# Performance work log

Measured on AMD Instinct MI355X. Metric: run time of the kernel, lower is better.

Reference implementation:

```python
import jax, jax.numpy as jnp
import numpy as np

B, S, IN, OUT = 4, 2048, 4096, 16384

def setup_inputs() -> dict:
    key = jax.random.key(0)
    k1, k2, k3, k4 = jax.random.split(key, 4)
    x = jax.random.normal(k1, (B, S, IN), dtype=jnp.float32)
    quantized_weight = jax.random.randint(k2, (OUT, IN), 0, 16, dtype=jnp.int32)
    scale = jax.random.uniform(k3, (OUT,), dtype=jnp.float32)
    zero_point = jax.random.randint(k4, (OUT,), 0, 16, dtype=jnp.int32)
    return {"x": x, "quantized_weight": quantized_weight, "scale": scale, "zero_point": zero_point}

def reference(x, quantized_weight, scale, zero_point):
    # Per-output-channel dequantization: W = (q - zp) * scale, shape [OUT, IN]
    weight = (quantized_weight.astype(jnp.float32) - zero_point.astype(jnp.float32)[:, None]) * scale[:, None]
    # F.linear(x, W) = x @ W.T -> [B, S, OUT]
    return jnp.einsum('bsi,oi->bso', x, weight)
```

## Files before the change

### kernel.cpp

```cpp
#include <hip/hip_runtime.h>
#include <stdint.h>

#define MDIM 8192
#define NDIM 16384
#define KDIM 4096
#define NT   64
#define PSTR 1048576

typedef __attribute__((ext_vector_type(4)))  int i32x4;
typedef __attribute__((ext_vector_type(16))) int i32x16;

__device__ __forceinline__ void gload_lds16(const void* g, void* l) {
    __builtin_amdgcn_global_load_lds(
        (const __attribute__((address_space(1))) void*)g,
        (__attribute__((address_space(3))) void*)l,
        16, 0, 0);
}

__device__ __forceinline__ i32x16 MFMA32(i32x4 a, i32x4 b, i32x16 c) {
    return __builtin_amdgcn_mfma_i32_32x32x32_i8(a, b, c, 0, 0, 0);
}


__global__ __launch_bounds__(256)
void rowmax_kernel(const float* __restrict__ x, float* __restrict__ sx,
                   float* __restrict__ invx) {
    const int row = (int)blockIdx.x;
    const float4* xr = (const float4*)(x + (long)row * KDIM);
    const int t = threadIdx.x;
    float m = 0.f;
#pragma unroll
    for (int i = 0; i < 4; ++i) {
        float4 v = xr[t + 256 * i];
        m = fmaxf(m, fmaxf(fmaxf(fabsf(v.x), fabsf(v.y)), fmaxf(fabsf(v.z), fabsf(v.w))));
    }
#pragma unroll
    for (int off = 32; off >= 1; off >>= 1) m = fmaxf(m, __shfl_xor(m, off));
    __shared__ float red[4];
    if ((t & 63) == 0) red[t >> 6] = m;
    __syncthreads();
    m = fmaxf(fmaxf(red[0], red[1]), fmaxf(red[2], red[3]));
    m = fmaxf(m, 1e-20f);
    if (t == 0) { sx[row] = m * (1.0f / 127.0f); invx[row] = 127.0f / m; }
}

__global__ __launch_bounds__(256)
void quantx_t2(const float* __restrict__ x, const float* __restrict__ invx,
               int8_t* __restrict__ xq) {
    __shared__ int4 tb[1024];
    const int b = (int)blockIdx.x;
    const int p = b >> 6, tt = b & 63;
    const int tid = threadIdx.x;
#pragma unroll
    for (int i = 0; i < 4; ++i) {
        const int idx = i * 256 + tid;
        const int row = idx >> 2, c = idx & 3;
        const float inv = invx[p * 256 + row];
        const float4* src = (const float4*)(x + ((long)p * 256 + row) * KDIM + tt * 64 + c * 16);
        union { int8_t ch[16]; int4 v; } r;
#pragma unroll
        for (int j = 0; j < 4; ++j) {
            float4 v = src[j];
            r.ch[j * 4 + 0] = (int8_t)__float2int_rn(v.x * inv);
            r.ch[j * 4 + 1] = (int8_t)__float2int_rn(v.y * inv);
            r.ch[j * 4 + 2] = (int8_t)__float2int_rn(v.z * inv);
            r.ch[j * 4 + 3] = (int8_t)__float2int_rn(v.w * inv);
        }
        tb[c * 256 + row] = r.v;
    }
    __syncthreads();
    int4* dst = (int4*)(xq + (long)p * PSTR + (long)tt * 16384);
#pragma unroll
    for (int i = 0; i < 4; ++i) {
        const int idx = i * 256 + tid;
        dst[idx] = tb[idx];
    }
}

__global__ __launch_bounds__(256)
void quantw_t2(const int* __restrict__ q, const int* __restrict__ zp,
               int8_t* __restrict__ wq) {
    __shared__ int4 tb[1024];
    const int b = (int)blockIdx.x;
    const int p = b >> 6, tt = b & 63;
    const int tid = threadIdx.x;
#pragma unroll
    for (int i = 0; i < 4; ++i) {
        const int idx = i * 256 + tid;
        const int row = idx >> 2, c = idx & 3;
        const int z = zp[p * 256 + row];
        const int4* src = (const int4*)(q + ((long)p * 256 + row) * KDIM + tt * 64 + c * 16);
        union { int8_t ch[16]; int4 v; } r;
#pragma unroll
        for (int j = 0; j < 4; ++j) {
            int4 a = src[j];
            r.ch[j * 4 + 0] = (int8_t)(a.x - z);
            r.ch[j * 4 + 1] = (int8_t)(a.y - z);
            r.ch[j * 4 + 2] = (int8_t)(a.z - z);
            r.ch[j * 4 + 3] = (int8_t)(a.w - z);
        }
        tb[c * 256 + row] = r.v;
    }
    __syncthreads();
    int4* dst = (int4*)(wq + (long)p * PSTR + (long)tt * 16384);
#pragma unroll
    for (int i = 0; i < 4; ++i) {
        const int idx = i * 256 + tid;
        dst[idx] = tb[idx];
    }
}


__global__ __launch_bounds__(256, 2)
void gemm_i8_kernel(const int8_t* __restrict__ A, const int8_t* __restrict__ Wt,
                    const float* __restrict__ scale, const float* __restrict__ sx,
                    float* __restrict__ C) {
    __shared__ int8_t lds[2][16384];

    const int wg  = (int)blockIdx.x;
    const int rr  = wg >> 9;
    const int ii  = wg & 511;
    const int bm2 = ii & 63;
    const int bn2 = rr * 8 + (ii >> 6);

    const int tid  = threadIdx.x;
    const int lane = tid & 63;
    const int wid  = tid >> 6;
    const int wm   = wid >> 1;
    const int wn   = wid & 1;
    const int l31  = lane & 31;
    const int lh   = lane >> 5;

    const int fA = lh * 2048 + (wm * 64 + l31) * 16;
    const int fB = 8192 + lh * 2048 + (wn * 64 + l31) * 16;

    const int s0 = tid, s1 = tid + 256;
    const int g0 = (s0 >> 7) * 4096 + (s0 & 127) * 16;
    const int g1 = (s1 >> 7) * 4096 + (s1 & 127) * 16;

    const int8_t* pA = A  + (long)(bm2 >> 1) * PSTR + (bm2 & 1) * 2048;
    const int8_t* pB = Wt + (long)(bn2 >> 1) * PSTR + (bn2 & 1) * 2048;

#define STAGE(BUF, TT)                                                              \
    do {                                                                            \
        const int ko_ = (TT) * 16384;                                               \
        gload_lds16(pA + ko_ + g0, &lds[BUF][s0 * 16]);                             \
        gload_lds16(pA + ko_ + g1, &lds[BUF][s1 * 16]);                             \
        gload_lds16(pB + ko_ + g0, &lds[BUF][8192 + s0 * 16]);                      \
        gload_lds16(pB + ko_ + g1, &lds[BUF][8192 + s1 * 16]);                      \
    } while (0)

    i32x16 acc[2][2];
#pragma unroll
    for (int i = 0; i < 2; ++i)
#pragma unroll
        for (int j = 0; j < 2; ++j)
#pragma unroll
            for (int r = 0; r < 16; ++r) acc[i][j][r] = 0;

    STAGE(0, 0);
    asm volatile("s_waitcnt vmcnt(0)" ::: "memory");
    __builtin_amdgcn_s_barrier();

    for (int t = 0; t < NT; ++t) {
        const int cur = t & 1;
        const bool pf = (t + 1 < NT);
        if (pf) STAGE(cur ^ 1, t + 1);

        i32x4 aF[4], bF[4];
#pragma unroll
        for (int mt = 0; mt < 2; ++mt)
#pragma unroll
            for (int ks = 0; ks < 2; ++ks)
                aF[mt * 2 + ks] = *(const i32x4*)&lds[cur][fA + ks * 4096 + mt * 512];
#pragma unroll
        for (int nt = 0; nt < 2; ++nt)
#pragma unroll
            for (int ks = 0; ks < 2; ++ks)
                bF[nt * 2 + ks] = *(const i32x4*)&lds[cur][fB + ks * 4096 + nt * 512];

        __builtin_amdgcn_s_setprio(1);
#pragma unroll
        for (int mt = 0; mt < 2; ++mt)
#pragma unroll
            for (int nt = 0; nt < 2; ++nt)
#pragma unroll
                for (int ks = 0; ks < 2; ++ks)
                    acc[mt][nt] = MFMA32(aF[mt * 2 + ks], bF[nt * 2 + ks], acc[mt][nt]);
        __builtin_amdgcn_s_setprio(0);

        asm volatile("s_waitcnt lgkmcnt(0)" ::: "memory");
        if (pf) asm volatile("s_waitcnt vmcnt(0)" ::: "memory");
        __builtin_amdgcn_s_barrier();
    }
#undef STAGE

    const long rowA0 = (long)bm2 * 128 + wm * 64;
    const int  colB0 = bn2 * 128 + wn * 64;
    float scj[2];
#pragma unroll
    for (int n = 0; n < 2; ++n) scj[n] = scale[colB0 + n * 32 + l31];
#pragma unroll
    for (int mt = 0; mt < 2; ++mt) {
#pragma unroll
        for (int g = 0; g < 4; ++g) {
            const long rb = rowA0 + mt * 32 + g * 8 + lh * 4;
            const float4 s4 = *(const float4*)(sx + rb);
#pragma unroll
            for (int n = 0; n < 2; ++n) {
                float* cp = C + rb * NDIM + colB0 + n * 32 + l31;
                cp[0 * (long)NDIM] = (float)acc[mt][n][g * 4 + 0] * scj[n] * s4.x;
                cp[1 * (long)NDIM] = (float)acc[mt][n][g * 4 + 1] * scj[n] * s4.y;
                cp[2 * (long)NDIM] = (float)acc[mt][n][g * 4 + 2] * scj[n] * s4.z;
                cp[3 * (long)NDIM] = (float)acc[mt][n][g * 4 + 3] * scj[n] * s4.w;
            }
        }
    }
}


__global__ __launch_bounds__(256)
void fallback_kernel(const float* __restrict__ x, const int* __restrict__ q,
                     const float* __restrict__ scale, const int* __restrict__ zp,
                     float* __restrict__ out) {
    __shared__ float sA[64][17];
    __shared__ float sB[64][17];
    const int bn = (int)blockIdx.x % (NDIM / 64);
    const int bm = (int)blockIdx.x / (NDIM / 64);
    const int t  = threadIdx.x;
    const int tx = t & 15, ty = t >> 4;
    const long rowA = (long)bm * 64, rowB = (long)bn * 64;
    float acc[4][4] = {};
    for (int k0 = 0; k0 < KDIM; k0 += 16) {
#pragma unroll
        for (int i = 0; i < 4; ++i) {
            const int e = t + i * 256;
            const int r = e >> 4, c = e & 15;
            sA[r][c] = x[(rowA + r) * KDIM + k0 + c];
            const int o = (int)rowB + r;
            sB[r][c] = (float)(q[(long)o * KDIM + k0 + c] - zp[o]) * scale[o];
        }
        __syncthreads();
#pragma unroll
        for (int kk = 0; kk < 16; ++kk) {
            float a[4], b[4];
#pragma unroll
            for (int i = 0; i < 4; ++i) a[i] = sA[ty * 4 + i][kk];
#pragma unroll
            for (int j = 0; j < 4; ++j) b[j] = sB[tx * 4 + j][kk];
#pragma unroll
            for (int i = 0; i < 4; ++i)
#pragma unroll
                for (int j = 0; j < 4; ++j) acc[i][j] += a[i] * b[j];
        }
        __syncthreads();
    }
#pragma unroll
    for (int i = 0; i < 4; ++i) {
        const long r = rowA + ty * 4 + i;
#pragma unroll
        for (int j = 0; j < 4; ++j)
            out[r * NDIM + rowB + tx * 4 + j] = acc[i][j];
    }
}


extern "C" void kernel_launch(void* const* d_in, const int* in_sizes, int n_in,
                              void* d_out, int out_size, void* d_ws, size_t ws_size,
                              hipStream_t stream) {
    const float* x     = (const float*)d_in[0];
    const int*   qw    = (const int*)d_in[1];
    const float* scale = (const float*)d_in[2];
    const int*   zp    = (const int*)d_in[3];
    float*       out   = (float*)d_out;

    const size_t needA  = (size_t)MDIM * KDIM;
    const size_t needW  = (size_t)NDIM * KDIM;
    const size_t needSx = (size_t)MDIM * sizeof(float);
    const size_t needIx = (size_t)MDIM * sizeof(float);

    if (ws_size >= needA + needW + needSx + needIx) {
        int8_t* xq = (int8_t*)d_ws;
        int8_t* wq = xq + needA;
        float*  sx = (float*)((char*)d_ws + needA + needW);
        float*  ix = sx + MDIM;
        rowmax_kernel<<<MDIM, 256, 0, stream>>>(x, sx, ix);
        quantx_t2<<<(MDIM / 256) * 64, 256, 0, stream>>>(x, ix, xq);
        quantw_t2<<<(NDIM / 256) * 64, 256, 0, stream>>>(qw, zp, wq);
        gemm_i8_kernel<<<(MDIM / 128) * (NDIM / 128), 256, 0, stream>>>(xq, wq, scale, sx, out);
    } else {
        fallback_kernel<<<(MDIM / 64) * (NDIM / 64), 256, 0, stream>>>(x, qw, scale, zp, out);
    }
}
```

Baseline: 811.7 us.

## Drop LDS staging, load MFMA fragments directly from global with 256x256 tiles

The int8 GEMM now uses 256x256 output tiles with 512 threads (8 waves as 2x4). It drops the LDS double buffer and global_load_lds staging: each wave loads its MFMA operand fragments straight from global memory into registers, ping-ponging between two register sets. This removes LDS traffic and block barriers. In exchange, operands shared between waves are fetched separately from global/L2 with no LDS sharing, and register pressure rises with 8 accumulators plus two fragment sets.

```diff
diff --git a/kernel.cpp b/kernel.cpp
--- a/kernel.cpp
+++ b/kernel.cpp
@@ -9,13 +9,6 @@
 
 typedef __attribute__((ext_vector_type(4)))  int i32x4;
 typedef __attribute__((ext_vector_type(16))) int i32x16;
-
-__device__ __forceinline__ void gload_lds16(const void* g, void* l) {
-    __builtin_amdgcn_global_load_lds(
-        (const __attribute__((address_space(1))) void*)g,
-        (__attribute__((address_space(3))) void*)l,
-        16, 0, 0);
-}
 
 __device__ __forceinline__ i32x16 MFMA32(i32x4 a, i32x4 b, i32x16 c) {
     return __builtin_amdgcn_mfma_i32_32x32x32_i8(a, b, c, 0, 0, 0);
@@ -111,97 +104,87 @@
 }
 
 
-__global__ __launch_bounds__(256, 2)
+__global__ __launch_bounds__(512, 2)
 void gemm_i8_kernel(const int8_t* __restrict__ A, const int8_t* __restrict__ Wt,
                     const float* __restrict__ scale, const float* __restrict__ sx,
                     float* __restrict__ C) {
-    __shared__ int8_t lds[2][16384];
-
-    const int wg  = (int)blockIdx.x;
-    const int rr  = wg >> 9;
-    const int ii  = wg & 511;
-    const int bm2 = ii & 63;
-    const int bn2 = rr * 8 + (ii >> 6);
+    const int wg = (int)blockIdx.x;
+    const int rr = wg >> 8;
+    const int ii = wg & 255;
+    const int bm = ii & 31;
+    const int bn = rr * 8 + (ii >> 5);
 
     const int tid  = threadIdx.x;
     const int lane = tid & 63;
     const int wid  = tid >> 6;
-    const int wm   = wid >> 1;
-    const int wn   = wid & 1;
+    const int wm   = wid >> 2;
+    const int wn   = wid & 3;
     const int l31  = lane & 31;
     const int lh   = lane >> 5;
 
-    const int fA = lh * 2048 + (wm * 64 + l31) * 16;
-    const int fB = 8192 + lh * 2048 + (wn * 64 + l31) * 16;
-
-    const int s0 = tid, s1 = tid + 256;
-    const int g0 = (s0 >> 7) * 4096 + (s0 & 127) * 16;
-    const int g1 = (s1 >> 7) * 4096 + (s1 & 127) * 16;
-
-    const int8_t* pA = A  + (long)(bm2 >> 1) * PSTR + (bm2 & 1) * 2048;
-    const int8_t* pB = Wt + (long)(bn2 >> 1) * PSTR + (bn2 & 1) * 2048;
-
-#define STAGE(BUF, TT)                                                              \
+    const int aoff = lh * 4096 + (wm * 128 + l31) * 16;
+    const int boff = lh * 4096 + (wn * 64 + l31) * 16;
+
+    const int8_t* pA = A  + (long)bm * PSTR;
+    const int8_t* pB = Wt + (long)bn * PSTR;
+
+#define LOADF(AS, BS, TT)                                                           \
     do {                                                                            \
-        const int ko_ = (TT) * 16384;                                               \
-        gload_lds16(pA + ko_ + g0, &lds[BUF][s0 * 16]);                             \
-        gload_lds16(pA + ko_ + g1, &lds[BUF][s1 * 16]);                             \
-        gload_lds16(pB + ko_ + g0, &lds[BUF][8192 + s0 * 16]);                      \
-        gload_lds16(pB + ko_ + g1, &lds[BUF][8192 + s1 * 16]);                      \
+        const int8_t* bA_ = pA + (TT) * 16384;                                      \
+        const int8_t* bB_ = pB + (TT) * 16384;                                      \
+        _Pragma("unroll")                                                           \
+        for (int mt_ = 0; mt_ < 4; ++mt_)                                           \
+            _Pragma("unroll")                                                       \
+            for (int ks_ = 0; ks_ < 2; ++ks_)                                       \
+                AS[mt_ * 2 + ks_] =                                                 \
+                    *(const i32x4*)(bA_ + ks_ * 8192 + mt_ * 512 + aoff);           \
+        _Pragma("unroll")                                                           \
+        for (int nt_ = 0; nt_ < 2; ++nt_)                                           \
+            _Pragma("unroll")                                                       \
+            for (int ks_ = 0; ks_ < 2; ++ks_)                                       \
+                BS[nt_ * 2 + ks_] =                                                 \
+                    *(const i32x4*)(bB_ + ks_ * 8192 + nt_ * 512 + boff);           \
     } while (0)
 
-    i32x16 acc[2][2];
-#pragma unroll
-    for (int i = 0; i < 2; ++i)
+#define MFMAALL(AS, BS)                                                             \
+    _Pragma("unroll")                                                               \
+    for (int mt_ = 0; mt_ < 4; ++mt_)                                               \
+        _Pragma("unroll")                                                           \
+        for (int nt_ = 0; nt_ < 2; ++nt_)                                           \
+            _Pragma("unroll")                                                       \
+            for (int ks_ = 0; ks_ < 2; ++ks_)                                       \
+                acc[mt_][nt_] = MFMA32(AS[mt_ * 2 + ks_], BS[nt_ * 2 + ks_],        \
+                                       acc[mt_][nt_]);
+
+    i32x16 acc[4][2];
+#pragma unroll
+    for (int i = 0; i < 4; ++i)
 #pragma unroll
         for (int j = 0; j < 2; ++j)
 #pragma unroll
             for (int r = 0; r < 16; ++r) acc[i][j][r] = 0;
 
-    STAGE(0, 0);
-    asm volatile("s_waitcnt vmcnt(0)" ::: "memory");
-    __builtin_amdgcn_s_barrier();
-
-    for (int t = 0; t < NT; ++t) {
-        const int cur = t & 1;
-        const bool pf = (t + 1 < NT);
-        if (pf) STAGE(cur ^ 1, t + 1);
-
-        i32x4 aF[4], bF[4];
-#pragma unroll
-        for (int mt = 0; mt < 2; ++mt)
-#pragma unroll
-            for (int ks = 0; ks < 2; ++ks)
-                aF[mt * 2 + ks] = *(const i32x4*)&lds[cur][fA + ks * 4096 + mt * 512];
-#pragma unroll
-        for (int nt = 0; nt < 2; ++nt)
-#pragma unroll
-            for (int ks = 0; ks < 2; ++ks)
-                bF[nt * 2 + ks] = *(const i32x4*)&lds[cur][fB + ks * 4096 + nt * 512];
-
-        __builtin_amdgcn_s_setprio(1);
-#pragma unroll
-        for (int mt = 0; mt < 2; ++mt)
-#pragma unroll
-            for (int nt = 0; nt < 2; ++nt)
-#pragma unroll
-                for (int ks = 0; ks < 2; ++ks)
-                    acc[mt][nt] = MFMA32(aF[mt * 2 + ks], bF[nt * 2 + ks], acc[mt][nt]);
-        __builtin_amdgcn_s_setprio(0);
-
-        asm volatile("s_waitcnt lgkmcnt(0)" ::: "memory");
-        if (pf) asm volatile("s_waitcnt vmcnt(0)" ::: "memory");
-        __builtin_amdgcn_s_barrier();
-    }
-#undef STAGE
-
-    const long rowA0 = (long)bm2 * 128 + wm * 64;
-    const int  colB0 = bn2 * 128 + wn * 64;
+    i32x4 aA[8], bA4[4], aB[8], bB4[4];
+
+    LOADF(aA, bA4, 0);
+    LOADF(aB, bB4, 1);
+
+    for (int t = 0; t < NT; t += 2) {
+        MFMAALL(aA, bA4);
+        if (t + 2 < NT) LOADF(aA, bA4, t + 2);
+        MFMAALL(aB, bB4);
+        if (t + 3 < NT) LOADF(aB, bB4, t + 3);
+    }
+#undef LOADF
+#undef MFMAALL
+
+    const long rowA0 = (long)bm * 256 + wm * 128;
+    const int  colB0 = bn * 256 + wn * 64;
     float scj[2];
 #pragma unroll
     for (int n = 0; n < 2; ++n) scj[n] = scale[colB0 + n * 32 + l31];
 #pragma unroll
-    for (int mt = 0; mt < 2; ++mt) {
+    for (int mt = 0; mt < 4; ++mt) {
 #pragma unroll
         for (int g = 0; g < 4; ++g) {
             const long rb = rowA0 + mt * 32 + g * 8 + lh * 4;
@@ -287,7 +270,7 @@
         rowmax_kernel<<<MDIM, 256, 0, stream>>>(x, sx, ix);
         quantx_t2<<<(MDIM / 256) * 64, 256, 0, stream>>>(x, ix, xq);
         quantw_t2<<<(NDIM / 256) * 64, 256, 0, stream>>>(qw, zp, wq);
-        gemm_i8_kernel<<<(MDIM / 128) * (NDIM / 128), 256, 0, stream>>>(xq, wq, scale, sx, out);
+        gemm_i8_kernel<<<(MDIM / 256) * (NDIM / 256), 512, 0, stream>>>(xq, wq, scale, sx, out);
     } else {
         fallback_kernel<<<(MDIM / 64) * (NDIM / 64), 256, 0, stream>>>(x, qw, scale, zp, out);
     }
```

Measured after the change: 801.8 us. Within noise of the previous version (-1.2%).
